# Optimization experiments

Hardware: AMD Instinct MI355X
Metric: run time of the kernel (lower is better)

Reference implementation:

```python
import jax, jax.numpy as jnp
import numpy as np

T, H = 8192, 2048          # num_tokens, hidden_size
NH, NKV, D = 16, 4, 128    # num_heads, num_kv_heads, head_dim
R = 16                     # gate_low_rank_dim
NORM = 16.0                # gate_logit_normalizer
EPS = 1e-6                 # RMSNorm eps


def setup_inputs() -> dict:
    key = jax.random.key(0)
    ks = jax.random.split(key, 8)
    rnd = lambda k, sh, f: jax.random.normal(k, sh, dtype=jnp.float32) * f
    return {
        "hidden_states": rnd(ks[0], (T, H), 1.0),
        "Wqkv": rnd(ks[1], (H, (NH + 2 * NKV) * D), 0.02),
        "bqkv": rnd(ks[2], ((NH + 2 * NKV) * D,), 0.02),
        "gk_w0": rnd(ks[3], (H, R), 0.02),
        "gk_w1": rnd(ks[4], (R, NKV * D), 0.02),
        "gk_b1": rnd(ks[5], (NKV * D,), 0.02),
        "gnorm_w": jnp.ones((D,), jnp.float32),
        "Wo": rnd(ks[6], (NH * D, H), 0.02),
    }


def _gla_scan(q, k, v, g):
    # q,k,v,g: [NH, T, D]. State S: [D, D] per head.
    def step(S, x):
        qt, kt, vt, gt = x
        S = jnp.exp(gt)[:, None] * S + kt[:, None] * vt[None, :]
        return S, qt @ S

    def per_head(qh, kh, vh, gh):
        S0 = jnp.zeros((D, D), qh.dtype)
        _, o = jax.lax.scan(step, S0, (qh, kh, vh, gh))
        return o  # [T, D]

    return jax.vmap(per_head)(q, k, v, g)  # [NH, T, D]


def reference(hidden_states, Wqkv, bqkv, gk_w0, gk_w1, gk_b1, gnorm_w, Wo):
    # qkv projection (with bias), split into q / k / v
    qkv = hidden_states @ Wqkv + bqkv                    # [T, (NH+2*NKV)*D]
    q, k, v = jnp.split(qkv, [NH * D, NH * D + NKV * D], axis=-1)
    # low-rank gate projection (bias0=False, bias1=True)
    gk = (hidden_states @ gk_w0) @ gk_w1 + gk_b1         # [T, NKV*D]

    q = jax.nn.relu(q).reshape(T, NH, D)                 # feature_map = relu
    k = jax.nn.relu(k).reshape(T, NKV, D)
    v = v.reshape(T, NKV, D)
    gk = jax.nn.log_sigmoid(gk).reshape(T, NKV, D) / NORM

    # GQA: repeat_interleave kv heads to NH heads
    rep = NH // NKV
    k = jnp.repeat(k, rep, axis=1)
    v = jnp.repeat(v, rep, axis=1)
    gk = jnp.repeat(gk, rep, axis=1)

    q = q * (D ** -0.5)                                  # fused_chunk_gla default scale

    qh, kh, vh, gh = (t.transpose(1, 0, 2) for t in (q, k, v, gk))  # [NH, T, D]
    o = _gla_scan(qh, kh, vh, gh)                        # [NH, T, D]

    # per-head RMSNorm over head_dim
    o = o * jax.lax.rsqrt(jnp.mean(o * o, axis=-1, keepdims=True) + EPS) * gnorm_w

    o = o.transpose(1, 0, 2).reshape(T, NH * D)          # h n d -> n (h d)
    return o @ Wo                                        # o_proj (no bias)
```

## Files before the change

kernel.cpp:

```cpp
#include <hip/hip_runtime.h>
#include <hip/hip_bf16.h>
#include <cstdint>

typedef unsigned short u16;
typedef unsigned int u32;
typedef float f32x4 __attribute__((ext_vector_type(4)));
typedef short bf16x8 __attribute__((ext_vector_type(8)));

#define T_TOK 8192
#define HID 2048
#define NH 16
#define NKV 4
#define HD 128
#define QKVN 3072
#define CHUNK 64
#define NC 128

__device__ __forceinline__ float bf2f(u16 h){
  u32 u = ((u32)h) << 16;
  return __builtin_bit_cast(float, u);
}
__device__ __forceinline__ u16 f2bf(float f){
  u32 u = __builtin_bit_cast(u32, f);
  u32 r = (u + 0x7fffu + ((u >> 16) & 1u)) >> 16;
  return (u16)r;
}
__device__ __forceinline__ u32 pack2(float a, float b){
  return (u32)f2bf(a) | ((u32)f2bf(b) << 16);
}
__device__ __forceinline__ void gl2lds16(const u16* g, u16* l){
  __builtin_amdgcn_global_load_lds(
      (const __attribute__((address_space(1))) u32*)g,
      (__attribute__((address_space(3))) u32*)l, 16, 0, 0);
}

__global__ __launch_bounds__(256) void cvt_f2b_kernel(
    const float* __restrict__ in, u16* __restrict__ out, int n8)
{
  int i = blockIdx.x*256 + threadIdx.x;
  if (i >= n8) return;
  const float4* p = (const float4*)(in + (size_t)i*8);
  float4 a = p[0], b = p[1];
  uint4 pk;
  pk.x = pack2(a.x, a.y); pk.y = pack2(a.z, a.w);
  pk.z = pack2(b.x, b.y); pk.w = pack2(b.z, b.w);
  *(uint4*)(out + (size_t)i*8) = pk;
}

#define BM 256
#define BN 256
#define BK 64
#define ABUF (BM*BK)
#define BBUF (BN*BK)
#define BUFU (ABUF + BBUF)

__device__ __forceinline__ int swz(int o){ return o ^ (((o >> 7) & 7) << 4); }

__device__ __forceinline__ void stage16(const u16* g, int ldg, u16* l, int o){
  int p = o ^ (((o >> 7) & 7) << 4);
  gl2lds16(g + (size_t)(p >> 7) * ldg + ((p >> 1) & 63), l + (o >> 1));
}

__device__ __forceinline__ void stage_half(const u16* g, int ldg, u16* lregion,
                                           int half, int tid){
  stage16(g, ldg, lregion, (half*1024 + tid)*16);
  stage16(g, ldg, lregion, (half*1024 + 512 + tid)*16);
}

template<typename YT>
__global__ __launch_bounds__(512, 2) void gemm_v2(
    const u16* __restrict__ X, const u16* __restrict__ Wt,
    const float* __restrict__ bias, const float* __restrict__ ebuf,
    const float* __restrict__ rbuf, YT* __restrict__ Y,
    int M, int N, int K, int mode)
{
  __shared__ u16 lds[2 * BUFU];
  const int tid  = threadIdx.x;
  const int lane = tid & 63;
  const int wave = tid >> 6;
  const int wm = wave >> 2;
  const int wn = wave & 3;
  const int ml = lane & 15, quad = lane >> 4;

  const int nwg = gridDim.x;
  const int chunk = nwg >> 3;
  const int lg = (blockIdx.x & 7) * chunk + (blockIdx.x >> 3);
  const int NBt = N >> 8;
  const int bm0 = (lg / NBt) * BM;
  const int bn0 = (lg % NBt) * BN;

  const u16* gA = X  + (size_t)bm0 * K;
  const u16* gB = Wt + (size_t)bn0 * K;

  f32x4 acc[8][4];
  #pragma unroll
  for (int i = 0; i < 8; i++)
    #pragma unroll
    for (int j = 0; j < 4; j++) acc[i][j] = f32x4{0.f, 0.f, 0.f, 0.f};

  const int NT = K >> 6;

  auto ldfrag = [&](const u16* base, int row, int kk)->bf16x8{
    return *(const bf16x8*)((const char*)base + swz(row*128 + kk*64 + quad*16));
  };

  {
    u16* La0 = lds;
    u16* Lb0 = lds + ABUF;
    stage_half(gB, K, Lb0, 0, tid);
    stage_half(gB, K, Lb0, 1, tid);
    stage_half(gA, K, La0, 0, tid);
    stage_half(gA, K, La0, 1, tid);
  }
  asm volatile("s_waitcnt vmcnt(2)" ::: "memory");
  __builtin_amdgcn_s_barrier();

  for (int t = 0; t < NT; ++t){
    u16* La = lds + (t & 1) * BUFU;
    u16* Lb = La + ABUF;
    u16* Na = lds + ((t + 1) & 1) * BUFU;
    u16* Nb = Na + ABUF;
    const u16* ga = gA + (t + 1) * BK;
    const u16* gb = gB + (t + 1) * BK;
    const bool st = (t + 1 < NT);

    #pragma unroll
    for (int kk = 0; kk < 2; ++kk){
      bf16x8 af[4], bfr[4];
      #pragma unroll
      for (int j = 0; j < 4; ++j) bfr[j] = ldfrag(Lb, wn*64 + j*16 + ml, kk);
      #pragma unroll
      for (int i = 0; i < 4; ++i) af[i] = ldfrag(La, wm*64 + i*16 + ml, kk);
      if (st){
        if (kk == 0) stage_half(gb, K, Nb, 0, tid);
        else         stage_half(ga, K, Na, 0, tid);
      }
      __builtin_amdgcn_sched_barrier(0);
      __builtin_amdgcn_s_barrier();
      asm volatile("s_waitcnt lgkmcnt(0)" ::: "memory");
      __builtin_amdgcn_sched_barrier(0);
      __builtin_amdgcn_s_setprio(1);
      #pragma unroll
      for (int i = 0; i < 4; ++i)
        #pragma unroll
        for (int j = 0; j < 4; ++j)
          acc[i][j] = __builtin_amdgcn_mfma_f32_16x16x32_bf16(af[i], bfr[j], acc[i][j], 0, 0, 0);
      __builtin_amdgcn_s_setprio(0);
      if (kk == 0){
        if (st) asm volatile("s_waitcnt vmcnt(2)" ::: "memory");
        else    asm volatile("s_waitcnt vmcnt(0)" ::: "memory");
      }
      __builtin_amdgcn_s_barrier();

      #pragma unroll
      for (int i = 0; i < 4; ++i) af[i] = ldfrag(La, 128 + wm*64 + i*16 + ml, kk);
      if (st){
        if (kk == 0) stage_half(gb, K, Nb, 1, tid);
        else         stage_half(ga, K, Na, 1, tid);
      }
      __builtin_amdgcn_sched_barrier(0);
      __builtin_amdgcn_s_barrier();
      asm volatile("s_waitcnt lgkmcnt(0)" ::: "memory");
      __builtin_amdgcn_sched_barrier(0);
      __builtin_amdgcn_s_setprio(1);
      #pragma unroll
      for (int i = 0; i < 4; ++i)
        #pragma unroll
        for (int j = 0; j < 4; ++j)
          acc[4+i][j] = __builtin_amdgcn_mfma_f32_16x16x32_bf16(af[i], bfr[j], acc[4+i][j], 0, 0, 0);
      __builtin_amdgcn_s_setprio(0);
      if (kk == 1 && st)
        asm volatile("s_waitcnt vmcnt(2)" ::: "memory");
      __builtin_amdgcn_s_barrier();
    }
  }

  #pragma unroll
  for (int rh = 0; rh < 2; rh++){
    #pragma unroll
    for (int i = 0; i < 4; i++){
      int row = bm0 + rh*128 + wm*64 + i*16 + quad*4;
      #pragma unroll
      for (int j = 0; j < 4; j++){
        int col = bn0 + wn*64 + j*16 + ml;
        float bv = 0.f;
        if (mode == 1) bv = bias[col];
        #pragma unroll
        for (int rr2 = 0; rr2 < 4; rr2++){
          float v = acc[rh*4+i][j][rr2] + bv;
          if (mode == 1){
            int token = row + rr2;
            int cc = token >> 6, tt = token & 63, ii = col & 127;
            if (col < 2048){
              v = fmaxf(v, 0.f) * 0.08838834764831845f;
              v *= ebuf[(((size_t)cc*4 + (col>>9))*64 + tt)*128 + ii];
            } else if (col < 2560){
              v = fmaxf(v, 0.f);
              v *= rbuf[(((size_t)cc*4 + ((col-2048)>>7))*64 + tt)*128 + ii];
            }
          }
          if (sizeof(YT) == 2) Y[(size_t)(row+rr2)*N + col] = (YT)f2bf(v);
          else                 Y[(size_t)(row+rr2)*N + col] = (YT)v;
        }
      }
    }
  }
}

__global__ __launch_bounds__(256) void transpose_f2b(
    const float* __restrict__ in, u16* __restrict__ out, int R, int C)
{
  __shared__ float tile[32][33];
  int c0 = blockIdx.x*32, r0 = blockIdx.y*32;
  int tx = threadIdx.x & 31, ty = threadIdx.x >> 5;
  #pragma unroll
  for (int p=0;p<4;p++) tile[ty + p*8][tx] = in[(size_t)(r0 + ty + p*8)*C + c0 + tx];
  __syncthreads();
  #pragma unroll
  for (int p=0;p<4;p++) out[(size_t)(c0 + ty + p*8)*R + r0 + tx] = f2bf(tile[tx][ty + p*8]);
}

__global__ __launch_bounds__(256) void gk1_kernel(
    const u16* __restrict__ hsb, const float* __restrict__ w0, float* __restrict__ tmp)
{
  int row = blockIdx.x*4 + (threadIdx.x >> 6);
  int lane = threadIdx.x & 63;
  float acc[16];
  #pragma unroll
  for (int n=0;n<16;n++) acc[n]=0.f;
  for (int k = lane; k < HID; k += 64){
    float h = bf2f(hsb[(size_t)row*HID + k]);
    const float* wr = w0 + (size_t)k*16;
    #pragma unroll
    for (int q=0;q<4;q++){
      float4 wv = *(const float4*)(wr + q*4);
      acc[q*4+0] += h*wv.x; acc[q*4+1] += h*wv.y;
      acc[q*4+2] += h*wv.z; acc[q*4+3] += h*wv.w;
    }
  }
  #pragma unroll
  for (int n=0;n<16;n++){
    #pragma unroll
    for (int off=32; off>0; off>>=1)
      acc[n] += __shfl_down(acc[n], off);
  }
  if (lane == 0){
    #pragma unroll
    for (int n=0;n<16;n++) tmp[(size_t)row*16 + n] = acc[n];
  }
}

__global__ __launch_bounds__(256) void gk2_kernel(
    const float* __restrict__ tmp, const float* __restrict__ w1,
    const float* __restrict__ b1, float* __restrict__ g)
{
  int id = blockIdx.x*256 + threadIdx.x;
  int rrow = id >> 9, n = id & 511;
  float a = b1[n];
  #pragma unroll
  for (int k=0;k<16;k++)
    a += tmp[(size_t)rrow*16 + k] * w1[k*512 + n];
  float ls = fminf(a, 0.f) - log1pf(__expf(-fabsf(a)));
  g[id] = ls * 0.0625f;
}

__global__ __launch_bounds__(256) void decay_kernel(
    const float* __restrict__ g, float* __restrict__ ebuf,
    float* __restrict__ rbuf, float* __restrict__ expB)
{
  __shared__ float bL[CHUNK*HD];
  const int c = blockIdx.x, h = blockIdx.y, tid = threadIdx.x;
  for (int off = tid; off < CHUNK*HD; off += 256){
    int t = off >> 7, i = off & 127;
    bL[off] = g[(size_t)(c*CHUNK + t)*512 + h*HD + i];
  }
  __syncthreads();
  if (tid < HD){
    float run = 0.f;
    for (int t=0;t<CHUNK;t++){ run += bL[t*HD + tid]; bL[t*HD + tid] = run; }
    expB[(size_t)(c*NKV + h)*HD + tid] = __expf(run);
  }
  __syncthreads();
  size_t base = (size_t)(c*NKV + h)*CHUNK*HD;
  for (int off = tid; off < CHUNK*HD; off += 256){
    float b = bL[off];
    ebuf[base + off] = __expf(b);
    rbuf[base + off] = __expf(-b);
  }
}

__global__ __launch_bounds__(256) void chunk_stats2_kernel(
    const u16* __restrict__ qkv, const float* __restrict__ expB,
    u16* __restrict__ Kt, u16* __restrict__ Vt)
{
  __shared__ u16 kL[CHUNK*HD];
  __shared__ u16 vL[CHUNK*HD];
  const int c = blockIdx.x, h = blockIdx.y, tid = threadIdx.x;
  #pragma unroll
  for (int it=0; it<4; it++){
    int u = it*256 + tid;
    int t = u >> 4, p = (u & 15)*8;
    size_t tok = (size_t)(c*CHUNK + t);
    *(uint4*)(kL + t*HD + p) = *(const uint4*)(qkv + tok*QKVN + 2048 + h*HD + p);
    *(uint4*)(vL + t*HD + p) = *(const uint4*)(qkv + tok*QKVN + 2560 + h*HD + p);
  }
  __syncthreads();
  {
    int j = tid >> 1, sh = (tid & 1)*32;
    u16* dst = Vt + ((size_t)(c*NKV + h)*HD + j)*CHUNK + sh;
    #pragma unroll
    for (int s2=0; s2<16; s2++){
      u32 a = (u32)vL[(sh + 2*s2)*HD + j] | ((u32)vL[(sh + 2*s2 + 1)*HD + j] << 16);
      *(u32*)(dst + 2*s2) = a;
    }
  }
  int jj = tid >> 1, ih = (tid & 1)*64;
  float acc[64];
  #pragma unroll
  for (int z=0;z<64;z++) acc[z]=0.f;
  for (int t=0;t<CHUNK;t++){
    float vj = bf2f(vL[t*HD + jj]);
    const u32* kp = (const u32*)(kL + t*HD + ih);
    #pragma unroll
    for (int z2=0; z2<32; z2++){
      u32 kw = kp[z2];
      acc[2*z2]   += vj * bf2f((u16)(kw & 0xffffu));
      acc[2*z2+1] += vj * bf2f((u16)(kw >> 16));
    }
  }
  u16* kout = Kt + ((size_t)(c*NKV + h)*HD + jj)*HD + ih;
  const float* eB = expB + (size_t)(c*NKV + h)*HD + ih;
  #pragma unroll
  for (int z2=0; z2<32; z2++)
    *(u32*)(kout + 2*z2) = pack2(acc[2*z2]*eB[2*z2], acc[2*z2+1]*eB[2*z2+1]);
}

__global__ __launch_bounds__(256) void state_scan2_kernel(
    const u16* __restrict__ Kt, const float* __restrict__ expB, u16* __restrict__ St)
{
  int wid = blockIdx.x;
  int h = wid >> 6;
  int j = (wid & 63)*2 + (threadIdx.x >> 7);
  int i = threadIdx.x & 127;
  size_t base = ((size_t)h*HD + j)*HD + i;
  float S = 0.f;
  for (int cc=0; cc<NC; cc++){
    size_t off = (size_t)cc*(NKV*HD*HD) + base;
    St[off] = f2bf(S);
    S = expB[((size_t)cc*NKV + h)*HD + i] * S + bf2f(Kt[off]);
  }
}

__global__ __launch_bounds__(256) void attn_fused_kernel(
    const u16* __restrict__ qkv, const u16* __restrict__ St,
    const u16* __restrict__ Vt, const float* __restrict__ gw,
    u16* __restrict__ obuf)
{
  __shared__ u16 qe[64*136];
  __shared__ u16 kb[64*136];
  __shared__ u16 sb[64*136];
  __shared__ u16 vb[128*72];
  __shared__ u16 pb[64*72];
  const int c = blockIdx.x, qh = blockIdx.y, h = qh >> 2;
  const int tid = threadIdx.x, lane = tid & 63, w = tid >> 6;
  const int ml = lane & 15, quad = lane >> 4, q8 = quad * 8;

  #pragma unroll
  for (int it = 0; it < 4; it++){
    int u = it*256 + tid;
    int t = u >> 4, p = (u & 15) * 8;
    size_t tok = (size_t)(c*CHUNK + t);
    *(uint4*)(qe + t*136 + p) = *(const uint4*)(qkv + tok*QKVN + qh*HD + p);
    *(uint4*)(kb + t*136 + p) = *(const uint4*)(qkv + tok*QKVN + 2048 + h*HD + p);
  }
  __syncthreads();

  bf16x8 aq[4];
  #pragma unroll
  for (int kk=0;kk<4;kk++)
    aq[kk] = *(const bf16x8*)(qe + (w*16 + ml)*136 + kk*32 + q8);
  #pragma unroll
  for (int n=0;n<4;n++){
    f32x4 pa = {0.f,0.f,0.f,0.f};
    #pragma unroll
    for (int kk=0;kk<4;kk++){
      bf16x8 bk = *(const bf16x8*)(kb + (n*16 + ml)*136 + kk*32 + q8);
      pa = __builtin_amdgcn_mfma_f32_16x16x32_bf16(aq[kk], bk, pa, 0, 0, 0);
    }
    #pragma unroll
    for (int r=0;r<4;r++){
      int ti = quad*4 + r;
      float v = (w*16 + ti >= n*16 + ml) ? pa[r] : 0.f;
      pb[(w*16 + ti)*72 + n*16 + ml] = f2bf(v);
    }
  }
  #pragma unroll
  for (int it = 0; it < 4; it++){
    int u = it*256 + tid;
    int j = u >> 3, p = (u & 7) * 8;
    *(uint4*)(vb + j*72 + p) =
        *(const uint4*)(Vt + ((size_t)(c*NKV + h)*HD + j)*CHUNK + p);
    int t2 = u >> 4, p2 = (u & 15) * 8;
    *(uint4*)(sb + t2*136 + p2) =
        *(const uint4*)(St + ((size_t)(c*NKV + h)*HD + t2)*HD + p2);
  }
  __syncthreads();

  f32x4 o[8];
  #pragma unroll
  for (int n=0;n<8;n++) o[n] = f32x4{0.f,0.f,0.f,0.f};
  bf16x8 ap[2];
  #pragma unroll
  for (int ks=0;ks<2;ks++)
    ap[ks] = *(const bf16x8*)(pb + (w*16 + ml)*72 + ks*32 + q8);
  #pragma unroll
  for (int n=0;n<8;n++)
    #pragma unroll
    for (int ks=0;ks<2;ks++){
      bf16x8 bv = *(const bf16x8*)(vb + (n*16 + ml)*72 + ks*32 + q8);
      o[n] = __builtin_amdgcn_mfma_f32_16x16x32_bf16(ap[ks], bv, o[n], 0, 0, 0);
    }
  #pragma unroll
  for (int n=0;n<4;n++)
    #pragma unroll
    for (int kk=0;kk<4;kk++){
      bf16x8 bs = *(const bf16x8*)(sb + (n*16 + ml)*136 + kk*32 + q8);
      o[n] = __builtin_amdgcn_mfma_f32_16x16x32_bf16(aq[kk], bs, o[n], 0, 0, 0);
    }
  #pragma unroll
  for (int it = 0; it < 4; it++){
    int u = it*256 + tid;
    int t2 = u >> 4, p2 = (u & 15) * 8;
    *(uint4*)(kb + t2*136 + p2) =
        *(const uint4*)(St + ((size_t)(c*NKV + h)*HD + 64 + t2)*HD + p2);
  }
  __syncthreads();
  #pragma unroll
  for (int n=0;n<4;n++)
    #pragma unroll
    for (int kk=0;kk<4;kk++){
      bf16x8 bs = *(const bf16x8*)(kb + (n*16 + ml)*136 + kk*32 + q8);
      o[4+n] = __builtin_amdgcn_mfma_f32_16x16x32_bf16(aq[kk], bs, o[4+n], 0, 0, 0);
    }

  float rstd[4];
  #pragma unroll
  for (int r=0;r<4;r++){
    float s = 0.f;
    #pragma unroll
    for (int n=0;n<8;n++) s += o[n][r]*o[n][r];
    #pragma unroll
    for (int off=1; off<16; off<<=1) s += __shfl_xor(s, off);
    rstd[r] = rsqrtf(s*(1.f/128.f) + 1e-6f);
  }
  #pragma unroll
  for (int n=0;n<8;n++){
    float gwv = gw[n*16 + ml];
    #pragma unroll
    for (int r=0;r<4;r++){
      int t = w*16 + quad*4 + r;
      float val = o[n][r] * rstd[r] * gwv;
      obuf[(size_t)(c*CHUNK + t)*(NH*HD) + qh*HD + n*16 + ml] = f2bf(val);
    }
  }
}

extern "C" void kernel_launch(void* const* d_in, const int* in_sizes, int n_in,
                              void* d_out, int out_size, void* d_ws, size_t ws_size,
                              hipStream_t stream)
{
  const float* hs   = (const float*)d_in[0];
  const float* Wqkv = (const float*)d_in[1];
  const float* bqkv = (const float*)d_in[2];
  const float* w0   = (const float*)d_in[3];
  const float* w1   = (const float*)d_in[4];
  const float* b1   = (const float*)d_in[5];
  const float* gw   = (const float*)d_in[6];
  const float* Wo   = (const float*)d_in[7];
  float* out = (float*)d_out;

  char* ws = (char*)d_ws;
  size_t off = 0;
  auto alloc = [&](size_t bytes)->char*{
    char* p = ws + off; off += (bytes + 255) & ~(size_t)255; return p;
  };
  u16*   hsb   = (u16*)  alloc((size_t)T_TOK*HID*2);
  u16*   Wt1   = (u16*)  alloc((size_t)QKVN*HID*2);
  u16*   Wt2   = (u16*)  alloc((size_t)HID*HID*2);
  u16*   qkv   = (u16*)  alloc((size_t)T_TOK*QKVN*2);
  float* gtmp  = (float*)alloc((size_t)T_TOK*16*4);
  float* g     = (float*)alloc((size_t)T_TOK*512*4);
  float* ebuf  = (float*)alloc((size_t)NC*NKV*CHUNK*HD*4);
  float* rbuf  = (float*)alloc((size_t)NC*NKV*CHUNK*HD*4);
  float* expB  = (float*)alloc((size_t)NC*NKV*HD*4);
  u16*   Kt    = (u16*)  alloc((size_t)NC*NKV*HD*HD*2);
  u16*   St    = (u16*)  alloc((size_t)NC*NKV*HD*HD*2);
  u16*   Vt    = (u16*)  alloc((size_t)NC*NKV*HD*CHUNK*2);
  u16*   obuf  = (u16*)  alloc((size_t)T_TOK*NH*HD*2);

  cvt_f2b_kernel<<<dim3(T_TOK*HID/8/256), 256, 0, stream>>>(hs, hsb, T_TOK*HID/8);
  transpose_f2b<<<dim3(QKVN/32, HID/32), 256, 0, stream>>>(Wqkv, Wt1, HID, QKVN);
  transpose_f2b<<<dim3(HID/32,  HID/32), 256, 0, stream>>>(Wo,   Wt2, HID, HID);
  gk1_kernel<<<dim3(T_TOK/4), 256, 0, stream>>>(hsb, w0, gtmp);
  gk2_kernel<<<dim3(T_TOK*512/256), 256, 0, stream>>>(gtmp, w1, b1, g);
  decay_kernel<<<dim3(NC, NKV), 256, 0, stream>>>(g, ebuf, rbuf, expB);
  gemm_v2<u16><<<dim3((T_TOK/BM)*(QKVN/BN)), 512, 0, stream>>>(
      hsb, Wt1, bqkv, ebuf, rbuf, qkv, T_TOK, QKVN, HID, 1);
  chunk_stats2_kernel<<<dim3(NC, NKV), 256, 0, stream>>>(qkv, expB, Kt, Vt);
  state_scan2_kernel<<<dim3(256), 256, 0, stream>>>(Kt, expB, St);
  attn_fused_kernel<<<dim3(NC, NH), 256, 0, stream>>>(qkv, St, Vt, gw, obuf);
  gemm_v2<float><<<dim3((T_TOK/BM)*(HID/BN)), 512, 0, stream>>>(
      obuf, Wt2, nullptr, nullptr, nullptr, out, T_TOK, HID, HID, 0);
}
```

Measured before the change: 600.4 us.

## Shrink GEMM tiles to 128x128 with 4 waves and k-split LDS planes

Replaces the 256x256, 512-thread GEMM with a 128x128, 256-thread variant. Each 64-wide K tile is split into two 32-wide LDS planes with a new 4-way XOR swizzle, and both A and B are staged per plane. Both the QKV and output projections use it, giving four times as many workgroups for better CU occupancy and wave balance. The cost is lower arithmetic intensity per tile and more global/L2 traffic.

```diff
diff --git a/kernel.cpp b/kernel.cpp
--- a/kernel.cpp
+++ b/kernel.cpp
@@ -47,93 +47,78 @@
   *(uint4*)(out + (size_t)i*8) = pk;
 }
 
-#define BM 256
-#define BN 256
 #define BK 64
-#define ABUF (BM*BK)
-#define BBUF (BN*BK)
-#define BUFU (ABUF + BBUF)
-
-__device__ __forceinline__ int swz(int o){ return o ^ (((o >> 7) & 7) << 4); }
-
-__device__ __forceinline__ void stage16(const u16* g, int ldg, u16* l, int o){
-  int p = o ^ (((o >> 7) & 7) << 4);
-  gl2lds16(g + (size_t)(p >> 7) * ldg + ((p >> 1) & 63), l + (o >> 1));
-}
-
-__device__ __forceinline__ void stage_half(const u16* g, int ldg, u16* lregion,
-                                           int half, int tid){
-  stage16(g, ldg, lregion, (half*1024 + tid)*16);
-  stage16(g, ldg, lregion, (half*1024 + 512 + tid)*16);
+
+__device__ __forceinline__ void stage_plane(const u16* gsrc, int ldg, u16* plane, int tid){
+  #pragma unroll
+  for (int l = 0; l < 2; ++l){
+    int o = l*4096 + tid*16;
+    int q = o ^ (((o >> 6) & 3) << 4);
+    gl2lds16(gsrc + (size_t)(q >> 6) * ldg + ((q & 63) >> 1), plane + (o >> 1));
+  }
 }
 
 template<typename YT>
-__global__ __launch_bounds__(512, 2) void gemm_v2(
+__global__ __launch_bounds__(256, 2) void gemm_v3(
     const u16* __restrict__ X, const u16* __restrict__ Wt,
     const float* __restrict__ bias, const float* __restrict__ ebuf,
     const float* __restrict__ rbuf, YT* __restrict__ Y,
     int M, int N, int K, int mode)
 {
-  __shared__ u16 lds[2 * BUFU];
+  __shared__ u16 lds[2 * 16384];
   const int tid  = threadIdx.x;
   const int lane = tid & 63;
   const int wave = tid >> 6;
-  const int wm = wave >> 2;
-  const int wn = wave & 3;
+  const int wm = wave >> 1;
+  const int wn = wave & 1;
   const int ml = lane & 15, quad = lane >> 4;
 
   const int nwg = gridDim.x;
   const int chunk = nwg >> 3;
   const int lg = (blockIdx.x & 7) * chunk + (blockIdx.x >> 3);
-  const int NBt = N >> 8;
-  const int bm0 = (lg / NBt) * BM;
-  const int bn0 = (lg % NBt) * BN;
+  const int NBt = N >> 7;
+  const int bm0 = (lg / NBt) * 128;
+  const int bn0 = (lg % NBt) * 128;
 
   const u16* gA = X  + (size_t)bm0 * K;
   const u16* gB = Wt + (size_t)bn0 * K;
 
-  f32x4 acc[8][4];
-  #pragma unroll
-  for (int i = 0; i < 8; i++)
+  f32x4 acc[4][4];
+  #pragma unroll
+  for (int i = 0; i < 4; i++)
     #pragma unroll
     for (int j = 0; j < 4; j++) acc[i][j] = f32x4{0.f, 0.f, 0.f, 0.f};
 
   const int NT = K >> 6;
 
-  auto ldfrag = [&](const u16* base, int row, int kk)->bf16x8{
-    return *(const bf16x8*)((const char*)base + swz(row*128 + kk*64 + quad*16));
+  auto ldfrag = [&](const u16* plane, int row)->bf16x8{
+    int b = row*64 + ((quad*16) ^ ((row & 3) << 4));
+    return *(const bf16x8*)((const char*)plane + b);
   };
 
-  {
-    u16* La0 = lds;
-    u16* Lb0 = lds + ABUF;
-    stage_half(gB, K, Lb0, 0, tid);
-    stage_half(gB, K, Lb0, 1, tid);
-    stage_half(gA, K, La0, 0, tid);
-    stage_half(gA, K, La0, 1, tid);
-  }
-  asm volatile("s_waitcnt vmcnt(2)" ::: "memory");
+  stage_plane(gA,      K, lds +     0, tid);
+  stage_plane(gB,      K, lds +  8192, tid);
+  stage_plane(gA + 32, K, lds +  4096, tid);
+  stage_plane(gB + 32, K, lds + 12288, tid);
+  asm volatile("s_waitcnt vmcnt(4)" ::: "memory");
   __builtin_amdgcn_s_barrier();
 
   for (int t = 0; t < NT; ++t){
-    u16* La = lds + (t & 1) * BUFU;
-    u16* Lb = La + ABUF;
-    u16* Na = lds + ((t + 1) & 1) * BUFU;
-    u16* Nb = Na + ABUF;
+    u16* Cb = lds + (t & 1) * 16384;
+    u16* Nb = lds + ((t + 1) & 1) * 16384;
     const u16* ga = gA + (t + 1) * BK;
     const u16* gb = gB + (t + 1) * BK;
     const bool st = (t + 1 < NT);
 
-    #pragma unroll
-    for (int kk = 0; kk < 2; ++kk){
-      bf16x8 af[4], bfr[4];
-      #pragma unroll
-      for (int j = 0; j < 4; ++j) bfr[j] = ldfrag(Lb, wn*64 + j*16 + ml, kk);
-      #pragma unroll
-      for (int i = 0; i < 4; ++i) af[i] = ldfrag(La, wm*64 + i*16 + ml, kk);
+    {
+      bf16x8 af[4], bfv[4];
+      #pragma unroll
+      for (int i = 0; i < 4; ++i) af[i]  = ldfrag(Cb,        wm*64 + i*16 + ml);
+      #pragma unroll
+      for (int j = 0; j < 4; ++j) bfv[j] = ldfrag(Cb + 8192, wn*64 + j*16 + ml);
       if (st){
-        if (kk == 0) stage_half(gb, K, Nb, 0, tid);
-        else         stage_half(ga, K, Na, 0, tid);
+        stage_plane(ga, K, Nb,        tid);
+        stage_plane(gb, K, Nb + 8192, tid);
       }
       __builtin_amdgcn_sched_barrier(0);
       __builtin_amdgcn_s_barrier();
@@ -144,19 +129,21 @@
       for (int i = 0; i < 4; ++i)
         #pragma unroll
         for (int j = 0; j < 4; ++j)
-          acc[i][j] = __builtin_amdgcn_mfma_f32_16x16x32_bf16(af[i], bfr[j], acc[i][j], 0, 0, 0);
+          acc[i][j] = __builtin_amdgcn_mfma_f32_16x16x32_bf16(af[i], bfv[j], acc[i][j], 0, 0, 0);
       __builtin_amdgcn_s_setprio(0);
-      if (kk == 0){
-        if (st) asm volatile("s_waitcnt vmcnt(2)" ::: "memory");
-        else    asm volatile("s_waitcnt vmcnt(0)" ::: "memory");
-      }
+      if (st) asm volatile("s_waitcnt vmcnt(4)" ::: "memory");
+      else    asm volatile("s_waitcnt vmcnt(0)" ::: "memory");
       __builtin_amdgcn_s_barrier();
-
-      #pragma unroll
-      for (int i = 0; i < 4; ++i) af[i] = ldfrag(La, 128 + wm*64 + i*16 + ml, kk);
+    }
+    {
+      bf16x8 af[4], bfv[4];
+      #pragma unroll
+      for (int i = 0; i < 4; ++i) af[i]  = ldfrag(Cb +  4096, wm*64 + i*16 + ml);
+      #pragma unroll
+      for (int j = 0; j < 4; ++j) bfv[j] = ldfrag(Cb + 12288, wn*64 + j*16 + ml);
       if (st){
-        if (kk == 0) stage_half(gb, K, Nb, 1, tid);
-        else         stage_half(ga, K, Na, 1, tid);
+        stage_plane(ga + 32, K, Nb +  4096, tid);
+        stage_plane(gb + 32, K, Nb + 12288, tid);
       }
       __builtin_amdgcn_sched_barrier(0);
       __builtin_amdgcn_s_barrier();
@@ -167,41 +154,37 @@
       for (int i = 0; i < 4; ++i)
         #pragma unroll
         for (int j = 0; j < 4; ++j)
-          acc[4+i][j] = __builtin_amdgcn_mfma_f32_16x16x32_bf16(af[i], bfr[j], acc[4+i][j], 0, 0, 0);
+          acc[i][j] = __builtin_amdgcn_mfma_f32_16x16x32_bf16(af[i], bfv[j], acc[i][j], 0, 0, 0);
       __builtin_amdgcn_s_setprio(0);
-      if (kk == 1 && st)
-        asm volatile("s_waitcnt vmcnt(2)" ::: "memory");
+      if (st) asm volatile("s_waitcnt vmcnt(4)" ::: "memory");
       __builtin_amdgcn_s_barrier();
     }
   }
 
   #pragma unroll
-  for (int rh = 0; rh < 2; rh++){
-    #pragma unroll
-    for (int i = 0; i < 4; i++){
-      int row = bm0 + rh*128 + wm*64 + i*16 + quad*4;
-      #pragma unroll
-      for (int j = 0; j < 4; j++){
-        int col = bn0 + wn*64 + j*16 + ml;
-        float bv = 0.f;
-        if (mode == 1) bv = bias[col];
-        #pragma unroll
-        for (int rr2 = 0; rr2 < 4; rr2++){
-          float v = acc[rh*4+i][j][rr2] + bv;
-          if (mode == 1){
-            int token = row + rr2;
-            int cc = token >> 6, tt = token & 63, ii = col & 127;
-            if (col < 2048){
-              v = fmaxf(v, 0.f) * 0.08838834764831845f;
-              v *= ebuf[(((size_t)cc*4 + (col>>9))*64 + tt)*128 + ii];
-            } else if (col < 2560){
-              v = fmaxf(v, 0.f);
-              v *= rbuf[(((size_t)cc*4 + ((col-2048)>>7))*64 + tt)*128 + ii];
-            }
+  for (int i = 0; i < 4; i++){
+    int row = bm0 + wm*64 + i*16 + quad*4;
+    #pragma unroll
+    for (int j = 0; j < 4; j++){
+      int col = bn0 + wn*64 + j*16 + ml;
+      float bv = 0.f;
+      if (mode == 1) bv = bias[col];
+      #pragma unroll
+      for (int rr2 = 0; rr2 < 4; rr2++){
+        float v = acc[i][j][rr2] + bv;
+        if (mode == 1){
+          int token = row + rr2;
+          int cc = token >> 6, tt = token & 63, ii = col & 127;
+          if (col < 2048){
+            v = fmaxf(v, 0.f) * 0.08838834764831845f;
+            v *= ebuf[(((size_t)cc*4 + (col>>9))*64 + tt)*128 + ii];
+          } else if (col < 2560){
+            v = fmaxf(v, 0.f);
+            v *= rbuf[(((size_t)cc*4 + ((col-2048)>>7))*64 + tt)*128 + ii];
           }
-          if (sizeof(YT) == 2) Y[(size_t)(row+rr2)*N + col] = (YT)f2bf(v);
-          else                 Y[(size_t)(row+rr2)*N + col] = (YT)v;
         }
+        if (sizeof(YT) == 2) Y[(size_t)(row+rr2)*N + col] = (YT)f2bf(v);
+        else                 Y[(size_t)(row+rr2)*N + col] = (YT)v;
       }
     }
   }
@@ -504,11 +487,11 @@
   gk1_kernel<<<dim3(T_TOK/4), 256, 0, stream>>>(hsb, w0, gtmp);
   gk2_kernel<<<dim3(T_TOK*512/256), 256, 0, stream>>>(gtmp, w1, b1, g);
   decay_kernel<<<dim3(NC, NKV), 256, 0, stream>>>(g, ebuf, rbuf, expB);
-  gemm_v2<u16><<<dim3((T_TOK/BM)*(QKVN/BN)), 512, 0, stream>>>(
+  gemm_v3<u16><<<dim3((T_TOK/128)*(QKVN/128)), 256, 0, stream>>>(
       hsb, Wt1, bqkv, ebuf, rbuf, qkv, T_TOK, QKVN, HID, 1);
   chunk_stats2_kernel<<<dim3(NC, NKV), 256, 0, stream>>>(qkv, expB, Kt, Vt);
   state_scan2_kernel<<<dim3(256), 256, 0, stream>>>(Kt, expB, St);
   attn_fused_kernel<<<dim3(NC, NH), 256, 0, stream>>>(qkv, St, Vt, gw, obuf);
-  gemm_v2<float><<<dim3((T_TOK/BM)*(HID/BN)), 512, 0, stream>>>(
+  gemm_v3<float><<<dim3((T_TOK/128)*(HID/128)), 256, 0, stream>>>(
       obuf, Wt2, nullptr, nullptr, nullptr, out, T_TOK, HID, HID, 0);
 }
```

Result: no change. 607.2 us (+1.1%).

## Replace QKV GEMM with 128x128-tile triple-buffered kernel

Applied to the files above, without the earlier changes.

Adds a new gemm_v4 kernel for the QKV projection that uses 128x128 output tiles, 256 threads, a 32-wide K step with a three-stage LDS ring buffer, and an XCD-aware block remap. The QKV launch moves from 256x256 tiles to this smaller tile, which gives more workgroups (1536 instead of 384) for better CU occupancy and load balance. In exchange, each tile reuses loaded data less, the LDS layout has no swizzle so bank conflicts are possible, and the earlier kernel's setprio and sched-barrier tuning is gone. The BK macro is renamed and the output projection still uses gemm_v2.

```diff
diff --git a/kernel.cpp b/kernel.cpp
--- a/kernel.cpp
+++ b/kernel.cpp
@@ -49,9 +49,9 @@
 
 #define BM 256
 #define BN 256
-#define BK 64
-#define ABUF (BM*BK)
-#define BBUF (BN*BK)
+#define BKV2 64
+#define ABUF (BM*BKV2)
+#define BBUF (BN*BKV2)
 #define BUFU (ABUF + BBUF)
 
 __device__ __forceinline__ int swz(int o){ return o ^ (((o >> 7) & 7) << 4); }
@@ -120,8 +120,8 @@
     u16* Lb = La + ABUF;
     u16* Na = lds + ((t + 1) & 1) * BUFU;
     u16* Nb = Na + ABUF;
-    const u16* ga = gA + (t + 1) * BK;
-    const u16* gb = gB + (t + 1) * BK;
+    const u16* ga = gA + (t + 1) * BKV2;
+    const u16* gb = gB + (t + 1) * BKV2;
     const bool st = (t + 1 < NT);
 
     #pragma unroll
@@ -207,6 +207,112 @@
   }
 }
 
+template<typename YT>
+__global__ __launch_bounds__(256) void gemm_v4(
+    const u16* __restrict__ X, const u16* __restrict__ Wt,
+    const float* __restrict__ bias, const float* __restrict__ ebuf,
+    const float* __restrict__ rbuf, YT* __restrict__ Y,
+    int M, int N, int K, int mode)
+{
+  __shared__ u16 lds[3 * 8192];
+  const int tid = threadIdx.x;
+  const int lane = tid & 63;
+  const int wave = tid >> 6;
+  const int wm = wave >> 1, wn = wave & 1;
+
+  const int nwg = gridDim.x;
+  const int chunk = nwg >> 3;
+  const int lg = (blockIdx.x & 7) * chunk + (blockIdx.x >> 3);
+  const int NBt = N >> 7;
+  const int bm0 = (lg / NBt) * 128;
+  const int bn0 = (lg % NBt) * 128;
+
+  f32x4 acc[4][4];
+  #pragma unroll
+  for (int i=0;i<4;i++)
+    #pragma unroll
+    for (int j=0;j<4;j++) acc[i][j] = f32x4{0.f,0.f,0.f,0.f};
+
+  const int row0 = tid >> 2, part8 = (tid & 3) * 8;
+  const int mrow = lane & 15, q8 = (lane >> 4) << 3;
+  const u16* xb = X  + (size_t)bm0 * K;
+  const u16* wb = Wt + (size_t)bn0 * K;
+
+  const int NT = K >> 5;
+
+  #pragma unroll
+  for (int tt = 0; tt < 2; ++tt){
+    u16* As = lds + tt * 8192;
+    u16* Bs = As + 4096;
+    int k0 = tt * 32;
+    #pragma unroll
+    for (int j=0;j<2;j++){
+      int rr = j*64 + row0;
+      gl2lds16(xb + (size_t)rr*K + k0 + part8, As + rr*32 + part8);
+      gl2lds16(wb + (size_t)rr*K + k0 + part8, Bs + rr*32 + part8);
+    }
+  }
+  asm volatile("s_waitcnt vmcnt(4)" ::: "memory");
+  __builtin_amdgcn_s_barrier();
+
+  for (int t = 0; t < NT; ++t){
+    u16* As = lds + (t % 3) * 8192;
+    u16* Bs = As + 4096;
+    if (t + 2 < NT){
+      u16* Ns = lds + ((t + 2) % 3) * 8192;
+      int k0 = (t + 2) * 32;
+      #pragma unroll
+      for (int j=0;j<2;j++){
+        int rr = j*64 + row0;
+        gl2lds16(xb + (size_t)rr*K + k0 + part8, Ns + rr*32 + part8);
+        gl2lds16(wb + (size_t)rr*K + k0 + part8, Ns + 4096 + rr*32 + part8);
+      }
+    }
+    bf16x8 af[4], bfr[4];
+    #pragma unroll
+    for (int i=0;i<4;i++){
+      af[i]  = *(const bf16x8*)(As + (wm*64 + i*16 + mrow)*32 + q8);
+      bfr[i] = *(const bf16x8*)(Bs + (wn*64 + i*16 + mrow)*32 + q8);
+    }
+    #pragma unroll
+    for (int i=0;i<4;i++)
+      #pragma unroll
+      for (int j=0;j<4;j++)
+        acc[i][j] = __builtin_amdgcn_mfma_f32_16x16x32_bf16(af[i], bfr[j], acc[i][j], 0, 0, 0);
+    if (t + 2 < NT)      asm volatile("s_waitcnt vmcnt(4)" ::: "memory");
+    else if (t + 1 < NT) asm volatile("s_waitcnt vmcnt(0)" ::: "memory");
+    __builtin_amdgcn_s_barrier();
+  }
+
+  #pragma unroll
+  for (int i=0;i<4;i++){
+    int row = bm0 + wm*64 + i*16 + (lane>>4)*4;
+    #pragma unroll
+    for (int j=0;j<4;j++){
+      int col = bn0 + wn*64 + j*16 + (lane&15);
+      float bv = 0.f;
+      if (mode == 1) bv = bias[col];
+      #pragma unroll
+      for (int rr2=0;rr2<4;rr2++){
+        float v = acc[i][j][rr2] + bv;
+        if (mode == 1){
+          int token = row + rr2;
+          int cc = token >> 6, tt = token & 63, ii = col & 127;
+          if (col < 2048){
+            v = fmaxf(v, 0.f) * 0.08838834764831845f;
+            v *= ebuf[(((size_t)cc*4 + (col>>9))*64 + tt)*128 + ii];
+          } else if (col < 2560){
+            v = fmaxf(v, 0.f);
+            v *= rbuf[(((size_t)cc*4 + ((col-2048)>>7))*64 + tt)*128 + ii];
+          }
+        }
+        if (sizeof(YT) == 2) Y[(size_t)(row+rr2)*N + col] = (YT)f2bf(v);
+        else                 Y[(size_t)(row+rr2)*N + col] = (YT)v;
+      }
+    }
+  }
+}
+
 __global__ __launch_bounds__(256) void transpose_f2b(
     const float* __restrict__ in, u16* __restrict__ out, int R, int C)
 {
@@ -504,7 +610,7 @@
   gk1_kernel<<<dim3(T_TOK/4), 256, 0, stream>>>(hsb, w0, gtmp);
   gk2_kernel<<<dim3(T_TOK*512/256), 256, 0, stream>>>(gtmp, w1, b1, g);
   decay_kernel<<<dim3(NC, NKV), 256, 0, stream>>>(g, ebuf, rbuf, expB);
-  gemm_v2<u16><<<dim3((T_TOK/BM)*(QKVN/BN)), 512, 0, stream>>>(
+  gemm_v4<u16><<<dim3((T_TOK/128)*(QKVN/128)), 256, 0, stream>>>(
       hsb, Wt1, bqkv, ebuf, rbuf, qkv, T_TOK, QKVN, HID, 1);
   chunk_stats2_kernel<<<dim3(NC, NKV), 256, 0, stream>>>(qkv, expB, Kt, Vt);
   state_scan2_kernel<<<dim3(256), 256, 0, stream>>>(Kt, expB, St);
```

New measurement: 557.3 us. 1.08x faster.
